# Performance work log

Hardware: AMD Instinct MI355X
Metric: run time of the kernel (lower is better)

Reference implementation:

```python
import jax, jax.numpy as jnp
import numpy as np

NUM_HEADS = 8  # matches init_kwargs

def setup_inputs() -> dict:
    key = jax.random.key(0)
    ks = jax.random.split(key, 5)
    b, n, c = 8, 4096, 512
    scale_in = 1.0 / np.sqrt(c)
    return {
        'x': jax.random.normal(ks[0], (b, n, c), jnp.float32),
        'wqkv_w': jax.random.normal(ks[1], (3 * c, c), jnp.float32) * scale_in,
        'wqkv_b': jax.random.normal(ks[2], (3 * c,), jnp.float32) * 0.02,
        'wp_w': jax.random.normal(ks[3], (c, c), jnp.float32) * scale_in,
        'wp_b': jax.random.normal(ks[4], (c,), jnp.float32) * 0.02,
    }

def reference(x, wqkv_w, wqkv_b, wp_w, wp_b):
    b, n, c = x.shape
    h = NUM_HEADS
    d = c // h
    # QKV projection (torch Linear: x @ W^T + b)
    qkv = x @ wqkv_w.T + wqkv_b                      # (b, n, 3c)
    qkv = jnp.transpose(qkv.reshape(b, n, 3, c), (2, 0, 1, 3))
    q, k, v = qkv[0], qkv[1], qkv[2]                 # each (b, n, c)
    # Faithful to original: reshape (b,n,h,d) -> (b,h,n,d) is a FLAT
    # reinterpretation (torch .reshape), not a transpose.
    q = q.reshape(b, n, h, d).reshape(b, h, n, d)
    k = k.reshape(b, n, h, d).reshape(b, h, n, d)
    v = v.reshape(b, n, h, d).reshape(b, h, n, d)
    # Channel (cross-covariance) attention: contract over tokens n.
    scores = jnp.einsum('bhnd,bhne->bhde', q, k) / jnp.sqrt(jnp.float32(d))
    weights = jax.nn.softmax(scores, axis=-1)        # softmax over head_dim
    y = jnp.einsum('bhde,bhme->bhdm', weights, v)    # (b, h, d, n)
    y = jnp.transpose(y, (0, 3, 1, 2)).reshape(b, n, c)
    return y @ wp_w.T + wp_b
```

## Files before the change

kernel.cpp:

```cpp
#include <hip/hip_runtime.h>

typedef short s16x8 __attribute__((ext_vector_type(8)));
typedef float f32x4 __attribute__((ext_vector_type(4)));
typedef unsigned short us;

__device__ inline us f2bf(float f){
    union{float f;unsigned u;} v{f};
    unsigned r = v.u + 0x7fff + ((v.u>>16)&1);
    return (us)(r>>16);
}

__device__ __forceinline__ void glds16(const us* g, us* l){
    __builtin_amdgcn_global_load_lds(
        (const __attribute__((address_space(1))) unsigned int*)(g),
        (__attribute__((address_space(3))) unsigned int*)(l), 16, 0, 0);
}

__global__ void cast_all(const float* __restrict__ x, const float* __restrict__ wqkv_w,
                         const float* __restrict__ wp_w, us* __restrict__ xbf,
                         us* __restrict__ wqkvbf, us* __restrict__ wpbf){
    int i = blockIdx.x*blockDim.x + threadIdx.x;
    const float* s; us* d; int j;
    if(i < 4194304){ s = x; d = xbf; j = i; }
    else if(i < 4390912){ s = wqkv_w; d = wqkvbf; j = i - 4194304; }
    else { s = wp_w; d = wpbf; j = i - 4390912; }
    float4 f = ((const float4*)s)[j];
    ushort4 o;
    o.x = f2bf(f.x); o.y = f2bf(f.y); o.z = f2bf(f.z); o.w = f2bf(f.w);
    ((ushort4*)d)[j] = o;
}

__launch_bounds__(256,4)
__global__ void gemm_qkv(const us* __restrict__ A, const us* __restrict__ B,
                         const float* __restrict__ bias, us* __restrict__ C){
    __shared__ __attribute__((aligned(16))) us sA[128*64];
    __shared__ __attribute__((aligned(16))) us sB[128*64];
    int t = threadIdx.x;
    int id = blockIdx.x;
    int xcd = id & 7, s = id >> 3;
    int nt = s % 12, mt = xcd*32 + s/12;
    int lane = t&63, wave = t>>6, quad = lane>>4, l15 = lane&15;
    int wm = wave>>1, wn = wave&1;

    int l8 = lane>>3;
    int sw = ((lane&7) ^ l8)*8;
    const us* Ag = A + (size_t)(mt*128 + wave*32 + l8)*512 + sw;
    const us* Bg = B + (size_t)(nt*128 + wave*32 + l8)*512 + sw;
    us* sAw = &sA[(wave*32)*64];
    us* sBw = &sB[(wave*32)*64];

    f32x4 acc[4][4];
    #pragma unroll
    for(int i=0;i<4;i++)
        #pragma unroll
        for(int j=0;j<4;j++) acc[i][j] = (f32x4){0.f,0.f,0.f,0.f};

    for(int k0=0; k0<512; k0+=64){
        glds16(Ag + k0,           sAw);
        glds16(Ag + 8*512 + k0,   sAw + 8*64);
        glds16(Ag + 16*512 + k0,  sAw + 16*64);
        glds16(Ag + 24*512 + k0,  sAw + 24*64);
        glds16(Bg + k0,           sBw);
        glds16(Bg + 8*512 + k0,   sBw + 8*64);
        glds16(Bg + 16*512 + k0,  sBw + 16*64);
        glds16(Bg + 24*512 + k0,  sBw + 24*64);
        __syncthreads();
        #pragma unroll
        for(int ks=0; ks<2; ks++){
            int kc = ks*4 + quad;
            s16x8 af[4], bfr[4];
            #pragma unroll
            for(int i=0;i<4;i++){
                int r = wm*64 + i*16 + l15;
                af[i] = *(const s16x8*)&sA[r*64 + ((kc ^ (r&7))<<3)];
            }
            #pragma unroll
            for(int j=0;j<4;j++){
                int r = wn*64 + j*16 + l15;
                bfr[j] = *(const s16x8*)&sB[r*64 + ((kc ^ (r&7))<<3)];
            }
            #pragma unroll
            for(int i=0;i<4;i++)
                #pragma unroll
                for(int j=0;j<4;j++)
                    acc[i][j] = __builtin_amdgcn_mfma_f32_16x16x32_bf16(bfr[j], af[i], acc[i][j], 0,0,0);
        }
        __syncthreads();
    }

    int row0 = mt*128 + wm*64, col0 = nt*128 + wn*64;
    float4 bv[4];
    #pragma unroll
    for(int j=0;j<4;j++) bv[j] = *(const float4*)&bias[col0 + j*16 + quad*4];
    #pragma unroll
    for(int i=0;i<4;i++){
        size_t rb = (size_t)(row0 + i*16 + l15)*1536 + col0;
        #pragma unroll
        for(int j=0;j<4;j++){
            ushort4 o;
            o.x = f2bf(acc[i][j][0] + bv[j].x);
            o.y = f2bf(acc[i][j][1] + bv[j].y);
            o.z = f2bf(acc[i][j][2] + bv[j].z);
            o.w = f2bf(acc[i][j][3] + bv[j].w);
            *(ushort4*)&C[rb + j*16 + quad*4] = o;
        }
    }
}

__launch_bounds__(256,4)
__global__ void attn_scores_mfma(const us* __restrict__ qkv, float* __restrict__ Sp){
    __shared__ __attribute__((aligned(16))) us sQt[64*72];
    __shared__ __attribute__((aligned(16))) us sKt[64*72];
    int t = threadIdx.x;
    int kb = blockIdx.x, head = blockIdx.y;
    int lane = t & 63, w = t >> 6;
    int quad = lane >> 4, l15 = lane & 15;
    int p = t & 31;
    int d0 = (t >> 5) * 8;

    f32x4 acc[4];
    #pragma unroll
    for(int j=0;j<4;j++) acc[j] = (f32x4){0.f,0.f,0.f,0.f};

    const us* gbase = qkv + (size_t)(head*512 + kb*64 + (p>>2))*1536 + (2*(p&3))*64 + d0;
    union U{uint4 v; us h[8];};
    U q0,q1,k0,k1, nq0,nq1,nk0,nk1;
    q0.v = *(const uint4*)gbase;         q1.v = *(const uint4*)(gbase + 64);
    k0.v = *(const uint4*)(gbase + 512); k1.v = *(const uint4*)(gbase + 576);

    #pragma unroll
    for(int c=0; c<8; c++){
        if(c<7){
            const us* g = gbase + (size_t)(c+1)*8*1536;
            nq0.v = *(const uint4*)g;         nq1.v = *(const uint4*)(g + 64);
            nk0.v = *(const uint4*)(g + 512); nk1.v = *(const uint4*)(g + 576);
        }
        #pragma unroll
        for(int j=0;j<8;j++){
            *(unsigned*)&sQt[(d0+j)*72 + 2*p] = (unsigned)q0.h[j] | ((unsigned)q1.h[j]<<16);
            *(unsigned*)&sKt[(d0+j)*72 + 2*p] = (unsigned)k0.h[j] | ((unsigned)k1.h[j]<<16);
        }
        __syncthreads();
        int d = w*16 + l15;
        #pragma unroll
        for(int ks=0; ks<2; ks++){
            int tb = ks*4 + quad;
            s16x8 af = *(const s16x8*)&sQt[d*72 + tb*8];
            #pragma unroll
            for(int jt=0; jt<4; jt++){
                s16x8 bfv = *(const s16x8*)&sKt[(jt*16+l15)*72 + tb*8];
                acc[jt] = __builtin_amdgcn_mfma_f32_16x16x32_bf16(af, bfv, acc[jt], 0,0,0);
            }
        }
        __syncthreads();
        q0 = nq0; q1 = nq1; k0 = nk0; k1 = nk1;
    }

    float* S = Sp + (size_t)(kb*64 + head)*4096;
    #pragma unroll
    for(int jt=0; jt<4; jt++){
        int e = jt*16 + l15;
        #pragma unroll
        for(int r=0; r<4; r++){
            int d = w*16 + quad*4 + r;
            S[d*64 + e] = acc[jt][r];
        }
    }
}

__launch_bounds__(256,2)
__global__ void softfold(const float* __restrict__ Sp, const us* __restrict__ wpbf,
                         us* __restrict__ Mcat){
    __shared__ us sWt[64*72];
    int t = threadIdx.x;
    int head = blockIdx.x>>2, part = blockIdx.x&3;
    int b = head>>3, h = head&7;
    int lane = t&63, w = t>>6, quad = lane>>4, l15 = lane&15;

    int d = t>>2, e0 = (t&3)*16;
    float vv[16];
    #pragma unroll
    for(int j=0;j<16;j++) vv[j] = 0.f;
    for(int kb=0; kb<8; kb++){
        const float4* pp = (const float4*)&Sp[(size_t)(kb*64 + head)*4096 + d*64 + e0];
        #pragma unroll
        for(int q=0;q<4;q++){
            float4 g = pp[q];
            vv[4*q+0]+=g.x; vv[4*q+1]+=g.y; vv[4*q+2]+=g.z; vv[4*q+3]+=g.w;
        }
    }
    float m = -1e30f;
    #pragma unroll
    for(int j=0;j<16;j++){ vv[j] *= 0.125f; m = fmaxf(m, vv[j]); }
    m = fmaxf(m, __shfl_xor(m, 1));
    m = fmaxf(m, __shfl_xor(m, 2));
    float ssum = 0.f;
    #pragma unroll
    for(int j=0;j<16;j++){ vv[j] = __expf(vv[j]-m); ssum += vv[j]; }
    ssum += __shfl_xor(ssum, 1);
    ssum += __shfl_xor(ssum, 2);
    float inv = 1.f/ssum;
    #pragma unroll
    for(int j=0;j<16;j++) sWt[(e0+j)*72 + d] = f2bf(vv[j]*inv);
    __syncthreads();

    #pragma unroll
    for(int i=0;i<2;i++){
        int nO = part*128 + w*32 + i*16 + l15;
        s16x8 af0 = *(const s16x8*)&wpbf[(size_t)nO*512 + h*64 + quad*8];
        s16x8 af1 = *(const s16x8*)&wpbf[(size_t)nO*512 + h*64 + 32 + quad*8];
        #pragma unroll
        for(int j=0;j<4;j++){
            s16x8 bf0 = *(const s16x8*)&sWt[(j*16+l15)*72 + quad*8];
            s16x8 bf1 = *(const s16x8*)&sWt[(j*16+l15)*72 + 32 + quad*8];
            f32x4 acc = (f32x4){0.f,0.f,0.f,0.f};
            acc = __builtin_amdgcn_mfma_f32_16x16x32_bf16(af0, bf0, acc, 0,0,0);
            acc = __builtin_amdgcn_mfma_f32_16x16x32_bf16(af1, bf1, acc, 0,0,0);
            #pragma unroll
            for(int r=0;r<4;r++){
                int row = part*128 + w*32 + i*16 + quad*4 + r;
                Mcat[((size_t)(b*512 + row))*512 + h*64 + j*16 + l15] = f2bf(acc[r]);
            }
        }
    }
}

__launch_bounds__(256,4)
__global__ void gemm_vout(const us* __restrict__ qkv, const us* __restrict__ Mcat,
                          const float* __restrict__ bias, float* __restrict__ out){
    __shared__ __attribute__((aligned(16))) us sA[128*64];
    __shared__ __attribute__((aligned(16))) us sB[128*64];
    int t = threadIdx.x;
    int id = blockIdx.x;
    int xcd = id & 7, s = id >> 3;
    int nt = s & 3, mt = xcd*32 + (s>>2);
    int b = mt>>5, mr = mt&31;
    int lane = t&63, wave = t>>6, quad = lane>>4, l15 = lane&15;
    int wm = wave>>1, wn = wave&1;

    int l8 = lane>>3;
    int sw = ((lane&7) ^ l8)*8;
    const us* Abase = qkv + ((size_t)(8*b)*512 + mr*16 + wave*4)*1536 + 1024 + l8*64 + sw;
    const us* Bbase = Mcat + ((size_t)(b*512 + nt*128 + wave*32 + l8))*512 + sw;
    us* sAw = &sA[(wave*32)*64];
    us* sBw = &sB[(wave*32)*64];

    f32x4 acc[4][4];
    #pragma unroll
    for(int i=0;i<4;i++)
        #pragma unroll
        for(int j=0;j<4;j++) acc[i][j] = (f32x4){0.f,0.f,0.f,0.f};

    for(int h=0; h<8; h++){
        const us* Ah = Abase + (size_t)h*512*1536;
        const us* Bh = Bbase + h*64;
        glds16(Ah,           sAw);
        glds16(Ah + 1536,    sAw + 8*64);
        glds16(Ah + 2*1536,  sAw + 16*64);
        glds16(Ah + 3*1536,  sAw + 24*64);
        glds16(Bh,           sBw);
        glds16(Bh + 8*512,   sBw + 8*64);
        glds16(Bh + 16*512,  sBw + 16*64);
        glds16(Bh + 24*512,  sBw + 24*64);
        __syncthreads();
        #pragma unroll
        for(int ks=0; ks<2; ks++){
            int kc = ks*4 + quad;
            s16x8 af[4], bfr[4];
            #pragma unroll
            for(int i=0;i<4;i++){
                int r = wm*64 + i*16 + l15;
                af[i] = *(const s16x8*)&sA[r*64 + ((kc ^ (r&7))<<3)];
            }
            #pragma unroll
            for(int j=0;j<4;j++){
                int r = wn*64 + j*16 + l15;
                bfr[j] = *(const s16x8*)&sB[r*64 + ((kc ^ (r&7))<<3)];
            }
            #pragma unroll
            for(int i=0;i<4;i++)
                #pragma unroll
                for(int j=0;j<4;j++)
                    acc[i][j] = __builtin_amdgcn_mfma_f32_16x16x32_bf16(bfr[j], af[i], acc[i][j], 0,0,0);
        }
        __syncthreads();
    }

    int row0 = b*4096 + mr*128 + wm*64;
    int col0 = nt*128 + wn*64;
    float4 bv[4];
    #pragma unroll
    for(int j=0;j<4;j++) bv[j] = *(const float4*)&bias[col0 + j*16 + quad*4];
    #pragma unroll
    for(int i=0;i<4;i++){
        size_t rb = (size_t)(row0 + i*16 + l15)*512 + col0;
        #pragma unroll
        for(int j=0;j<4;j++){
            float4 o;
            o.x = acc[i][j][0] + bv[j].x;
            o.y = acc[i][j][1] + bv[j].y;
            o.z = acc[i][j][2] + bv[j].z;
            o.w = acc[i][j][3] + bv[j].w;
            *(float4*)&out[rb + j*16 + quad*4] = o;
        }
    }
}

extern "C" void kernel_launch(void* const* d_in, const int* in_sizes, int n_in,
                              void* d_out, int out_size, void* d_ws, size_t ws_size,
                              hipStream_t stream){
    const float* x      = (const float*)d_in[0];
    const float* wqkv_w = (const float*)d_in[1];
    const float* wqkv_b = (const float*)d_in[2];
    const float* wp_w   = (const float*)d_in[3];
    const float* wp_b   = (const float*)d_in[4];

    char* ws = (char*)d_ws;
    us*    qkvbf  = (us*)(ws);
    us*    xbf    = (us*)(ws + 100663296);
    float* Spart  = (float*)(ws + 134217728);
    us*    Mcat   = (us*)(ws + 143130624);
    us*    wqkvbf = (us*)(ws + 147324928);
    us*    wpbf   = (us*)(ws + 148897792);

    cast_all<<<17408,256,0,stream>>>(x, wqkv_w, wp_w, xbf, wqkvbf, wpbf);

    gemm_qkv<<<3072,256,0,stream>>>(xbf, wqkvbf, wqkv_b, qkvbf);

    attn_scores_mfma<<<dim3(8,64),256,0,stream>>>(qkvbf, Spart);
    softfold<<<256,256,0,stream>>>(Spart, wpbf, Mcat);

    gemm_vout<<<1024,256,0,stream>>>(qkvbf, Mcat, wp_b, (float*)d_out);
}
```

Before: 242.6 us.

## Fuse x fp32-to-bf16 cast into QKV GEMM A-tile loads

The separate cast of x to bf16 is removed. The QKV GEMM now loads fp32 x tiles straight into LDS and converts them to bf16 with packed cvt instructions while building MFMA fragments. This drops a full read and write pass over the 64 MB activation, but doubles LDS use and A-tile load traffic in the GEMM, and x is re-read by each of the 12 column tiles, so launch bounds drop to 3 blocks per CU. The attention scores kernel also loses its register prefetch double-buffering in favour of simple per-chunk loads.

New measurement: 258.6 us. +6.6%, slower.

```diff
diff --git a/kernel.cpp b/kernel.cpp
--- a/kernel.cpp
+++ b/kernel.cpp
@@ -15,25 +15,37 @@
         (const __attribute__((address_space(1))) unsigned int*)(g),
         (__attribute__((address_space(3))) unsigned int*)(l), 16, 0, 0);
 }
-
-__global__ void cast_all(const float* __restrict__ x, const float* __restrict__ wqkv_w,
-                         const float* __restrict__ wp_w, us* __restrict__ xbf,
-                         us* __restrict__ wqkvbf, us* __restrict__ wpbf){
+__device__ __forceinline__ void glds16f(const float* g, float* l){
+    __builtin_amdgcn_global_load_lds(
+        (const __attribute__((address_space(1))) unsigned int*)(g),
+        (__attribute__((address_space(3))) unsigned int*)(l), 16, 0, 0);
+}
+
+__device__ __forceinline__ s16x8 cvt8(const float4 lo, const float4 hi){
+    union{unsigned u[4]; s16x8 v;} o;
+    asm("v_cvt_pk_bf16_f32 %0, %1, %2" : "=v"(o.u[0]) : "v"(lo.x), "v"(lo.y));
+    asm("v_cvt_pk_bf16_f32 %0, %1, %2" : "=v"(o.u[1]) : "v"(lo.z), "v"(lo.w));
+    asm("v_cvt_pk_bf16_f32 %0, %1, %2" : "=v"(o.u[2]) : "v"(hi.x), "v"(hi.y));
+    asm("v_cvt_pk_bf16_f32 %0, %1, %2" : "=v"(o.u[3]) : "v"(hi.z), "v"(hi.w));
+    return o.v;
+}
+
+__global__ void cast_w(const float* __restrict__ wqkv_w, const float* __restrict__ wp_w,
+                       us* __restrict__ wqkvbf, us* __restrict__ wpbf){
     int i = blockIdx.x*blockDim.x + threadIdx.x;
     const float* s; us* d; int j;
-    if(i < 4194304){ s = x; d = xbf; j = i; }
-    else if(i < 4390912){ s = wqkv_w; d = wqkvbf; j = i - 4194304; }
-    else { s = wp_w; d = wpbf; j = i - 4390912; }
+    if(i < 196608){ s = wqkv_w; d = wqkvbf; j = i; }
+    else { s = wp_w; d = wpbf; j = i - 196608; }
     float4 f = ((const float4*)s)[j];
     ushort4 o;
     o.x = f2bf(f.x); o.y = f2bf(f.y); o.z = f2bf(f.z); o.w = f2bf(f.w);
     ((ushort4*)d)[j] = o;
 }
 
-__launch_bounds__(256,4)
-__global__ void gemm_qkv(const us* __restrict__ A, const us* __restrict__ B,
+__launch_bounds__(256,3)
+__global__ void gemm_qkv(const float* __restrict__ X, const us* __restrict__ B,
                          const float* __restrict__ bias, us* __restrict__ C){
-    __shared__ __attribute__((aligned(16))) us sA[128*64];
+    __shared__ __attribute__((aligned(16))) float sAf[128*64];
     __shared__ __attribute__((aligned(16))) us sB[128*64];
     int t = threadIdx.x;
     int id = blockIdx.x;
@@ -42,12 +54,16 @@
     int lane = t&63, wave = t>>6, quad = lane>>4, l15 = lane&15;
     int wm = wave>>1, wn = wave&1;
 
+    int l16r = lane>>4;
+    int sl = lane&15;
+    int swzA = (sl ^ (2*l16r)) << 2;
+    const float* Ae = X + (size_t)(mt*128 + wave*32 + l16r)*512 + swzA;
+    const float* Ao = X + (size_t)(mt*128 + wave*32 + l16r)*512 + (swzA ^ 32);
     int l8 = lane>>3;
-    int sw = ((lane&7) ^ l8)*8;
-    const us* Ag = A + (size_t)(mt*128 + wave*32 + l8)*512 + sw;
-    const us* Bg = B + (size_t)(nt*128 + wave*32 + l8)*512 + sw;
-    us* sAw = &sA[(wave*32)*64];
-    us* sBw = &sB[(wave*32)*64];
+    int swB = ((lane&7) ^ l8)*8;
+    const us* Bg = B + (size_t)(nt*128 + wave*32 + l8)*512 + swB;
+    float* sAw = &sAf[(wave*32)*64];
+    us*    sBw = &sB[(wave*32)*64];
 
     f32x4 acc[4][4];
     #pragma unroll
@@ -56,10 +72,11 @@
         for(int j=0;j<4;j++) acc[i][j] = (f32x4){0.f,0.f,0.f,0.f};
 
     for(int k0=0; k0<512; k0+=64){
-        glds16(Ag + k0,           sAw);
-        glds16(Ag + 8*512 + k0,   sAw + 8*64);
-        glds16(Ag + 16*512 + k0,  sAw + 16*64);
-        glds16(Ag + 24*512 + k0,  sAw + 24*64);
+        #pragma unroll
+        for(int r=0;r<8;r++){
+            const float* src = (r&1) ? Ao : Ae;
+            glds16f(src + (size_t)r*4*512 + k0, sAw + r*4*64);
+        }
         glds16(Bg + k0,           sBw);
         glds16(Bg + 8*512 + k0,   sBw + 8*64);
         glds16(Bg + 16*512 + k0,  sBw + 16*64);
@@ -72,7 +89,8 @@
             #pragma unroll
             for(int i=0;i<4;i++){
                 int r = wm*64 + i*16 + l15;
-                af[i] = *(const s16x8*)&sA[r*64 + ((kc ^ (r&7))<<3)];
+                const float* p = &sAf[r*64 + ((kc ^ (r&7))<<3)];
+                af[i] = cvt8(*(const float4*)p, *(const float4*)(p+4));
             }
             #pragma unroll
             for(int j=0;j<4;j++){
@@ -122,19 +140,12 @@
     #pragma unroll
     for(int j=0;j<4;j++) acc[j] = (f32x4){0.f,0.f,0.f,0.f};
 
-    const us* gbase = qkv + (size_t)(head*512 + kb*64 + (p>>2))*1536 + (2*(p&3))*64 + d0;
-    union U{uint4 v; us h[8];};
-    U q0,q1,k0,k1, nq0,nq1,nk0,nk1;
-    q0.v = *(const uint4*)gbase;         q1.v = *(const uint4*)(gbase + 64);
-    k0.v = *(const uint4*)(gbase + 512); k1.v = *(const uint4*)(gbase + 576);
-
-    #pragma unroll
-    for(int c=0; c<8; c++){
-        if(c<7){
-            const us* g = gbase + (size_t)(c+1)*8*1536;
-            nq0.v = *(const uint4*)g;         nq1.v = *(const uint4*)(g + 64);
-            nk0.v = *(const uint4*)(g + 512); nk1.v = *(const uint4*)(g + 576);
-        }
+    for(int chunk=0; chunk<8; chunk++){
+        int r0 = head*512 + kb*64 + chunk*8;
+        const us* g = qkv + (size_t)(r0 + (p>>2))*1536 + (2*(p&3))*64 + d0;
+        union{uint4 v; us h[8];} q0, q1, k0, k1;
+        q0.v = *(const uint4*)g;         q1.v = *(const uint4*)(g + 64);
+        k0.v = *(const uint4*)(g + 512); k1.v = *(const uint4*)(g + 576);
         #pragma unroll
         for(int j=0;j<8;j++){
             *(unsigned*)&sQt[(d0+j)*72 + 2*p] = (unsigned)q0.h[j] | ((unsigned)q1.h[j]<<16);
@@ -148,12 +159,12 @@
             s16x8 af = *(const s16x8*)&sQt[d*72 + tb*8];
             #pragma unroll
             for(int jt=0; jt<4; jt++){
-                s16x8 bfv = *(const s16x8*)&sKt[(jt*16+l15)*72 + tb*8];
+                int e = jt*16 + l15;
+                s16x8 bfv = *(const s16x8*)&sKt[e*72 + tb*8];
                 acc[jt] = __builtin_amdgcn_mfma_f32_16x16x32_bf16(af, bfv, acc[jt], 0,0,0);
             }
         }
         __syncthreads();
-        q0 = nq0; q1 = nq1; k0 = nk0; k1 = nk1;
     }
 
     float* S = Sp + (size_t)(kb*64 + head)*4096;
@@ -317,15 +328,14 @@
 
     char* ws = (char*)d_ws;
     us*    qkvbf  = (us*)(ws);
-    us*    xbf    = (us*)(ws + 100663296);
     float* Spart  = (float*)(ws + 134217728);
     us*    Mcat   = (us*)(ws + 143130624);
     us*    wqkvbf = (us*)(ws + 147324928);
     us*    wpbf   = (us*)(ws + 148897792);
 
-    cast_all<<<17408,256,0,stream>>>(x, wqkv_w, wp_w, xbf, wqkvbf, wpbf);
-
-    gemm_qkv<<<3072,256,0,stream>>>(xbf, wqkvbf, wqkv_b, qkvbf);
+    cast_w<<<1024,256,0,stream>>>(wqkv_w, wp_w, wqkvbf, wpbf);
+
+    gemm_qkv<<<3072,256,0,stream>>>(x, wqkvbf, wqkv_b, qkvbf);
 
     attn_scores_mfma<<<dim3(8,64),256,0,stream>>>(qkvbf, Spart);
     softfold<<<256,256,0,stream>>>(Spart, wpbf, Mcat);
```

## Overlap next-tile global-to-LDS loads with last MFMA half in GEMM kernels

Applied to the files above, without the earlier changes.

In the QKV and output projection GEMMs, the first tile load is hoisted before the loop. Each iteration loads its second k-half fragments into registers, syncs, issues the async global_load_lds for the next tile, and then runs the remaining MFMAs, so the memory fetch overlaps compute on a single LDS buffer. Separately, the attention score kernel drops its register prefetch of the next chunk and loads each chunk inline, which lowers register pressure but exposes that load latency. The overlap costs extra fragment registers and is limited to half an iteration of MFMA work.

After: 255.8 us. +5.4%, slower.

```diff
diff --git a/kernel.cpp b/kernel.cpp
--- a/kernel.cpp
+++ b/kernel.cpp
@@ -55,19 +55,19 @@
         #pragma unroll
         for(int j=0;j<4;j++) acc[i][j] = (f32x4){0.f,0.f,0.f,0.f};
 
+    glds16(Ag,           sAw);
+    glds16(Ag + 8*512,   sAw + 8*64);
+    glds16(Ag + 16*512,  sAw + 16*64);
+    glds16(Ag + 24*512,  sAw + 24*64);
+    glds16(Bg,           sBw);
+    glds16(Bg + 8*512,   sBw + 8*64);
+    glds16(Bg + 16*512,  sBw + 16*64);
+    glds16(Bg + 24*512,  sBw + 24*64);
+
     for(int k0=0; k0<512; k0+=64){
-        glds16(Ag + k0,           sAw);
-        glds16(Ag + 8*512 + k0,   sAw + 8*64);
-        glds16(Ag + 16*512 + k0,  sAw + 16*64);
-        glds16(Ag + 24*512 + k0,  sAw + 24*64);
-        glds16(Bg + k0,           sBw);
-        glds16(Bg + 8*512 + k0,   sBw + 8*64);
-        glds16(Bg + 16*512 + k0,  sBw + 16*64);
-        glds16(Bg + 24*512 + k0,  sBw + 24*64);
         __syncthreads();
-        #pragma unroll
-        for(int ks=0; ks<2; ks++){
-            int kc = ks*4 + quad;
+        {
+            int kc = quad;
             s16x8 af[4], bfr[4];
             #pragma unroll
             for(int i=0;i<4;i++){
@@ -85,7 +85,37 @@
                 for(int j=0;j<4;j++)
                     acc[i][j] = __builtin_amdgcn_mfma_f32_16x16x32_bf16(bfr[j], af[i], acc[i][j], 0,0,0);
         }
-        __syncthreads();
+        s16x8 af1[4], bfr1[4];
+        {
+            int kc = 4 + quad;
+            #pragma unroll
+            for(int i=0;i<4;i++){
+                int r = wm*64 + i*16 + l15;
+                af1[i] = *(const s16x8*)&sA[r*64 + ((kc ^ (r&7))<<3)];
+            }
+            #pragma unroll
+            for(int j=0;j<4;j++){
+                int r = wn*64 + j*16 + l15;
+                bfr1[j] = *(const s16x8*)&sB[r*64 + ((kc ^ (r&7))<<3)];
+            }
+        }
+        if(k0 < 448){
+            __syncthreads();
+            int kn = k0 + 64;
+            glds16(Ag + kn,           sAw);
+            glds16(Ag + 8*512 + kn,   sAw + 8*64);
+            glds16(Ag + 16*512 + kn,  sAw + 16*64);
+            glds16(Ag + 24*512 + kn,  sAw + 24*64);
+            glds16(Bg + kn,           sBw);
+            glds16(Bg + 8*512 + kn,   sBw + 8*64);
+            glds16(Bg + 16*512 + kn,  sBw + 16*64);
+            glds16(Bg + 24*512 + kn,  sBw + 24*64);
+        }
+        #pragma unroll
+        for(int i=0;i<4;i++)
+            #pragma unroll
+            for(int j=0;j<4;j++)
+                acc[i][j] = __builtin_amdgcn_mfma_f32_16x16x32_bf16(bfr1[j], af1[i], acc[i][j], 0,0,0);
     }
 
     int row0 = mt*128 + wm*64, col0 = nt*128 + wn*64;
@@ -122,19 +152,12 @@
     #pragma unroll
     for(int j=0;j<4;j++) acc[j] = (f32x4){0.f,0.f,0.f,0.f};
 
-    const us* gbase = qkv + (size_t)(head*512 + kb*64 + (p>>2))*1536 + (2*(p&3))*64 + d0;
-    union U{uint4 v; us h[8];};
-    U q0,q1,k0,k1, nq0,nq1,nk0,nk1;
-    q0.v = *(const uint4*)gbase;         q1.v = *(const uint4*)(gbase + 64);
-    k0.v = *(const uint4*)(gbase + 512); k1.v = *(const uint4*)(gbase + 576);
-
-    #pragma unroll
-    for(int c=0; c<8; c++){
-        if(c<7){
-            const us* g = gbase + (size_t)(c+1)*8*1536;
-            nq0.v = *(const uint4*)g;         nq1.v = *(const uint4*)(g + 64);
-            nk0.v = *(const uint4*)(g + 512); nk1.v = *(const uint4*)(g + 576);
-        }
+    for(int chunk=0; chunk<8; chunk++){
+        int r0 = head*512 + kb*64 + chunk*8;
+        const us* g = qkv + (size_t)(r0 + (p>>2))*1536 + (2*(p&3))*64 + d0;
+        union{uint4 v; us h[8];} q0, q1, k0, k1;
+        q0.v = *(const uint4*)g;         q1.v = *(const uint4*)(g + 64);
+        k0.v = *(const uint4*)(g + 512); k1.v = *(const uint4*)(g + 576);
         #pragma unroll
         for(int j=0;j<8;j++){
             *(unsigned*)&sQt[(d0+j)*72 + 2*p] = (unsigned)q0.h[j] | ((unsigned)q1.h[j]<<16);
@@ -148,12 +171,12 @@
             s16x8 af = *(const s16x8*)&sQt[d*72 + tb*8];
             #pragma unroll
             for(int jt=0; jt<4; jt++){
-                s16x8 bfv = *(const s16x8*)&sKt[(jt*16+l15)*72 + tb*8];
+                int e = jt*16 + l15;
+                s16x8 bfv = *(const s16x8*)&sKt[e*72 + tb*8];
                 acc[jt] = __builtin_amdgcn_mfma_f32_16x16x32_bf16(af, bfv, acc[jt], 0,0,0);
             }
         }
         __syncthreads();
-        q0 = nq0; q1 = nq1; k0 = nk0; k1 = nk1;
     }
 
     float* S = Sp + (size_t)(kb*64 + head)*4096;
@@ -251,21 +274,19 @@
         #pragma unroll
         for(int j=0;j<4;j++) acc[i][j] = (f32x4){0.f,0.f,0.f,0.f};
 
+    glds16(Abase,           sAw);
+    glds16(Abase + 1536,    sAw + 8*64);
+    glds16(Abase + 2*1536,  sAw + 16*64);
+    glds16(Abase + 3*1536,  sAw + 24*64);
+    glds16(Bbase,           sBw);
+    glds16(Bbase + 8*512,   sBw + 8*64);
+    glds16(Bbase + 16*512,  sBw + 16*64);
+    glds16(Bbase + 24*512,  sBw + 24*64);
+
     for(int h=0; h<8; h++){
-        const us* Ah = Abase + (size_t)h*512*1536;
-        const us* Bh = Bbase + h*64;
-        glds16(Ah,           sAw);
-        glds16(Ah + 1536,    sAw + 8*64);
-        glds16(Ah + 2*1536,  sAw + 16*64);
-        glds16(Ah + 3*1536,  sAw + 24*64);
-        glds16(Bh,           sBw);
-        glds16(Bh + 8*512,   sBw + 8*64);
-        glds16(Bh + 16*512,  sBw + 16*64);
-        glds16(Bh + 24*512,  sBw + 24*64);
         __syncthreads();
-        #pragma unroll
-        for(int ks=0; ks<2; ks++){
-            int kc = ks*4 + quad;
+        {
+            int kc = quad;
             s16x8 af[4], bfr[4];
             #pragma unroll
             for(int i=0;i<4;i++){
@@ -283,7 +304,38 @@
                 for(int j=0;j<4;j++)
                     acc[i][j] = __builtin_amdgcn_mfma_f32_16x16x32_bf16(bfr[j], af[i], acc[i][j], 0,0,0);
         }
-        __syncthreads();
+        s16x8 af1[4], bfr1[4];
+        {
+            int kc = 4 + quad;
+            #pragma unroll
+            for(int i=0;i<4;i++){
+                int r = wm*64 + i*16 + l15;
+                af1[i] = *(const s16x8*)&sA[r*64 + ((kc ^ (r&7))<<3)];
+            }
+            #pragma unroll
+            for(int j=0;j<4;j++){
+                int r = wn*64 + j*16 + l15;
+                bfr1[j] = *(const s16x8*)&sB[r*64 + ((kc ^ (r&7))<<3)];
+            }
+        }
+        if(h < 7){
+            __syncthreads();
+            const us* Ah = Abase + (size_t)(h+1)*512*1536;
+            const us* Bh = Bbase + (h+1)*64;
+            glds16(Ah,           sAw);
+            glds16(Ah + 1536,    sAw + 8*64);
+            glds16(Ah + 2*1536,  sAw + 16*64);
+            glds16(Ah + 3*1536,  sAw + 24*64);
+            glds16(Bh,           sBw);
+            glds16(Bh + 8*512,   sBw + 8*64);
+            glds16(Bh + 16*512,  sBw + 16*64);
+            glds16(Bh + 24*512,  sBw + 24*64);
+        }
+        #pragma unroll
+        for(int i=0;i<4;i++)
+            #pragma unroll
+            for(int j=0;j<4;j++)
+                acc[i][j] = __builtin_amdgcn_mfma_f32_16x16x32_bf16(bfr1[j], af1[i], acc[i][j], 0,0,0);
     }
 
     int row0 = b*4096 + mr*128 + wm*64;
```
